# Performance work log

Measured on AMD Instinct MI355X. Metric: run time of the kernel, lower is better.

The kernel has to match this reference:

```python
import jax, jax.numpy as jnp
import numpy as np

N_NODES = 50000
NEG_SLOPE = 0.2


def _gat_conv(x, src, dst, W, a_src, a_dst, b, num_nodes):
    # W: [H*C, F_in]; a_src/a_dst: [H, C]; b: [H*C]
    H, C = a_src.shape
    xp = (x @ W.T).reshape(num_nodes, H, C)              # [N,H,C]
    alpha_s = jnp.sum(xp * a_src[None], axis=-1)          # [N,H]
    alpha_d = jnp.sum(xp * a_dst[None], axis=-1)          # [N,H]
    e = jax.nn.leaky_relu(alpha_s[src] + alpha_d[dst], NEG_SLOPE)  # [E,H]
    # segment softmax over incoming edges of each dst node (self-loops guarantee non-empty segments)
    m = jax.ops.segment_max(e, dst, num_segments=num_nodes)
    e = jnp.exp(e - m[dst])
    s = jax.ops.segment_sum(e, dst, num_segments=num_nodes)
    alpha = e / s[dst]                                    # [E,H]
    out = jax.ops.segment_sum(alpha[:, :, None] * xp[src], dst, num_segments=num_nodes)  # [N,H,C]
    return out.reshape(num_nodes, H * C) + b


def setup_inputs() -> dict:
    key = jax.random.key(0)
    ks = jax.random.split(key, 12)
    N, E, F_in, HID, H, Z = N_NODES, 800000, 128, 64, 2, 32
    sc = 0.1
    return {
        "features": jax.random.normal(ks[0], (N, F_in), jnp.float32),
        "edges": jax.random.randint(ks[1], (2, E), 0, N, jnp.int32),
        "W1": jax.random.normal(ks[2], (H * HID, F_in), jnp.float32) * sc,
        "a_src1": jax.random.normal(ks[3], (H, HID), jnp.float32) * sc,
        "a_dst1": jax.random.normal(ks[4], (H, HID), jnp.float32) * sc,
        "b1": jnp.zeros((H * HID,), jnp.float32),
        "W_mu": jax.random.normal(ks[5], (Z, H * HID), jnp.float32) * sc,
        "a_src_mu": jax.random.normal(ks[6], (1, Z), jnp.float32) * sc,
        "a_dst_mu": jax.random.normal(ks[7], (1, Z), jnp.float32) * sc,
        "b_mu": jnp.zeros((Z,), jnp.float32),
        "W_std": jax.random.normal(ks[8], (Z, H * HID), jnp.float32) * sc,
        "a_src_std": jax.random.normal(ks[9], (1, Z), jnp.float32) * sc,
        "a_dst_std": jax.random.normal(ks[10], (1, Z), jnp.float32) * sc,
        "b_std": jnp.zeros((Z,), jnp.float32),
    }


def reference(features, edges, W1, a_src1, a_dst1, b1, W_mu, a_src_mu, a_dst_mu, b_mu, W_std, a_src_std, a_dst_std, b_std):
    N = features.shape[0]
    loops = jnp.arange(N, dtype=edges.dtype)
    src = jnp.concatenate([edges[0], loops])  # add self loops (PyG default)
    dst = jnp.concatenate([edges[1], loops])
    h = _gat_conv(features, src, dst, W1, a_src1, a_dst1, b1, N)
    h = jax.nn.relu(h)  # dropout p=0.0 -> identity
    mu = _gat_conv(h, src, dst, W_mu, a_src_mu, a_dst_mu, b_mu, N)
    std = _gat_conv(h, src, dst, W_std, a_src_std, a_dst_std, b_std, N)
    return (mu, std)
```

## Files before the change

### kernel.cpp

```cpp
#include <hip/hip_runtime.h>
#include <math.h>

#define N_NODES 50000
#define N_EDGES 800000
#define ET (N_EDGES + N_NODES)
#define KD 128
#define Z 32
#define SH 7
#define BW 128
#define NBUCK ((N_NODES + BW - 1) / BW)
#define CHUNK 4096
#define NBLKA ((ET + CHUNK - 1) / CHUNK)
#define MTOT (NBUCK * NBLKA)
#define MBS ((MTOT + 1023) / 1024)

typedef __attribute__((ext_vector_type(8))) short bf16x8;
typedef __attribute__((ext_vector_type(4))) float f32x4;

static __device__ __forceinline__ float lrelu(float x){ return x > 0.f ? x : 0.2f*x; }
static __device__ __forceinline__ float bf2f(unsigned int u16){ return __uint_as_float(u16 << 16); }
static __device__ __forceinline__ float lof(unsigned int u){ return __uint_as_float(u << 16); }
static __device__ __forceinline__ float hif(unsigned int u){ return __uint_as_float(u & 0xffff0000u); }
static __device__ __forceinline__ unsigned short f2bf(float f){
  unsigned int x = __float_as_uint(f);
  return (unsigned short)((x + 0x7fffu + ((x >> 16) & 1u)) >> 16);
}

__global__ __launch_bounds__(256) void bhistA_kernel(const int* __restrict__ edges, int* __restrict__ M){
  int k = blockIdx.x, t = threadIdx.x;
  __shared__ int cnt[NBUCK];
  for(int b = t; b < NBUCK; b += 256) cnt[b] = 0;
  __syncthreads();
  int base = k*CHUNK;
  int lim = min(base + CHUNK, ET);
  for(int i = base + t; i < lim; i += 256){
    int d = (i < N_EDGES) ? edges[N_EDGES + i] : (i - N_EDGES);
    atomicAdd(&cnt[d >> SH], 1);
  }
  __syncthreads();
  for(int b = t; b < NBUCK; b += 256) M[b*NBLKA + k] = cnt[b];
}

__global__ __launch_bounds__(256) void scanM1_kernel(const int* __restrict__ M, int* __restrict__ bsumM){
  int b = blockIdx.x, t = threadIdx.x;
  int base = b*1024 + t*4;
  int s = 0;
  #pragma unroll
  for(int i=0;i<4;i++){ int n = base+i; if(n < MTOT) s += M[n]; }
  for(int off=32; off; off>>=1) s += __shfl_xor(s, off);
  __shared__ int ws[4];
  if((t&63)==0) ws[t>>6] = s;
  __syncthreads();
  if(t==0) bsumM[b] = ws[0]+ws[1]+ws[2]+ws[3];
}

__global__ __launch_bounds__(256) void scanM2_kernel(const int* __restrict__ bsumM, int* __restrict__ bpreM){
  __shared__ int sm[256];
  int t = threadIdx.x;
  int v = (t < MBS) ? bsumM[t] : 0;
  sm[t] = v;
  __syncthreads();
  for(int off=1; off<256; off<<=1){
    int u = (t >= off) ? sm[t-off] : 0;
    __syncthreads();
    sm[t] += u;
    __syncthreads();
  }
  if(t < MBS) bpreM[t] = sm[t] - v;
}

__global__ __launch_bounds__(256) void scanM3_kernel(const int* __restrict__ M, const int* __restrict__ bpreM,
                                                     int* __restrict__ Mpos){
  int b = blockIdx.x, t = threadIdx.x;
  int lane = t & 63, wv = t >> 6;
  int base = b*1024 + t*4;
  int d[4]; int s = 0;
  #pragma unroll
  for(int i=0;i<4;i++){ int n = base+i; d[i] = (n < MTOT) ? M[n] : 0; s += d[i]; }
  int v = s;
  for(int off=1; off<64; off<<=1){
    int u = __shfl_up(v, off);
    if(lane >= off) v += u;
  }
  int texcl = v - s;
  __shared__ int wtot[4];
  if(lane == 63) wtot[wv] = v;
  __syncthreads();
  int woff = 0;
  for(int i=0;i<wv;i++) woff += wtot[i];
  int run = bpreM[b] + woff + texcl;
  #pragma unroll
  for(int i=0;i<4;i++){
    int n = base+i;
    if(n < MTOT){ Mpos[n] = run; run += d[i]; }
  }
}

__global__ __launch_bounds__(256) void bplaceA_kernel(const int* __restrict__ edges, const int* __restrict__ Mpos,
                                                      int2* __restrict__ etmp){
  int k = blockIdx.x, t = threadIdx.x;
  __shared__ int cur[NBUCK];
  for(int b = t; b < NBUCK; b += 256) cur[b] = Mpos[b*NBLKA + k];
  __syncthreads();
  int base = k*CHUNK;
  int lim = min(base + CHUNK, ET);
  for(int i = base + t; i < lim; i += 256){
    int s, d;
    if(i < N_EDGES){ s = edges[i]; d = edges[N_EDGES+i]; } else { s = d = i - N_EDGES; }
    int pos = atomicAdd(&cur[d >> SH], 1);
    etmp[pos] = make_int2(s, d);
  }
}

__global__ __launch_bounds__(256) void bfin_kernel(const int* __restrict__ Mpos, const int2* __restrict__ etmp,
                                                   int* __restrict__ rowptr, int* __restrict__ esrc){
  int b = blockIdx.x, t = threadIdx.x;
  __shared__ int cnt[BW];
  __shared__ int pre[BW];
  __shared__ int lcur[BW];
  if(t < BW) cnt[t] = 0;
  __syncthreads();
  int beg = Mpos[b*NBLKA];
  int end = (b+1 < NBUCK) ? Mpos[(b+1)*NBLKA] : ET;
  for(int i = beg + t; i < end; i += 256) atomicAdd(&cnt[etmp[i].y & (BW-1)], 1);
  __syncthreads();
  if(t < BW) pre[t] = cnt[t];
  __syncthreads();
  for(int off=1; off<BW; off<<=1){
    int u = 0;
    if(t < BW && t >= off) u = pre[t-off];
    __syncthreads();
    if(t < BW) pre[t] += u;
    __syncthreads();
  }
  if(t < BW){
    int excl = pre[t] - cnt[t];
    int node = b*BW + t;
    if(node < N_NODES) rowptr[node] = beg + excl;
    lcur[t] = beg + excl;
  }
  if(b == 0 && t == 255) rowptr[N_NODES] = ET;
  __syncthreads();
  for(int i = beg + t; i < end; i += 256){
    int2 e = etmp[i];
    int pos = atomicAdd(&lcur[e.y & (BW-1)], 1);
    esrc[pos] = e.x;
  }
}

__global__ __launch_bounds__(256) void wconv_kernel(const float* __restrict__ W1,
                                                    const float* __restrict__ Wmu, const float* __restrict__ Wst,
                                                    unsigned short* __restrict__ Wb1, unsigned short* __restrict__ Wb2){
  int i = blockIdx.x*256 + threadIdx.x;
  if(i < 128*KD) Wb1[i] = f2bf(W1[i]);
  if(i < 64*KD) Wb2[i] = f2bf(i < 32*KD ? Wmu[i] : Wst[i - 32*KD]);
}

__global__ __launch_bounds__(256) void mmt1_kernel(const float* __restrict__ X,
                                                   const unsigned short* __restrict__ Wb,
                                                   const float* __restrict__ asv, const float* __restrict__ adv,
                                                   unsigned short* __restrict__ outb,
                                                   float* __restrict__ as1, float* __restrict__ ad1){
  constexpr int OC = 128, CT = 8;
  int t = threadIdx.x;
  int w = t >> 6, L = t & 63;
  int col = L & 15, quad = L >> 4;
  int row0 = blockIdx.x*64 + w*16;
  int rA = row0 + col;
  if(rA >= N_NODES) rA = N_NODES-1;

  f32x4 acc[CT];
  #pragma unroll
  for(int ct=0;ct<CT;ct++) acc[ct] = (f32x4){0.f,0.f,0.f,0.f};

  #pragma unroll
  for(int kc=0;kc<4;kc++){
    int k0 = kc*32 + quad*8;
    const float* Xf = X + (size_t)rA*KD + k0;
    float4 p = *(const float4*)Xf;
    float4 q = *(const float4*)(Xf + 4);
    bf16x8 a;
    a[0] = (short)f2bf(p.x); a[1] = (short)f2bf(p.y);
    a[2] = (short)f2bf(p.z); a[3] = (short)f2bf(p.w);
    a[4] = (short)f2bf(q.x); a[5] = (short)f2bf(q.y);
    a[6] = (short)f2bf(q.z); a[7] = (short)f2bf(q.w);
    #pragma unroll
    for(int ct=0;ct<CT;ct++){
      bf16x8 b = *(const bf16x8*)(Wb + (size_t)(ct*16 + col)*KD + k0);
      acc[ct] = __builtin_amdgcn_mfma_f32_16x16x32_bf16(a, b, acc[ct], 0, 0, 0);
    }
  }

  float av[CT], dv[CT];
  #pragma unroll
  for(int ct=0;ct<CT;ct++){ av[ct] = asv[ct*16 + col]; dv[ct] = adv[ct*16 + col]; }

  #pragma unroll
  for(int r=0;r<4;r++){
    int row = row0 + quad*4 + r;
    #pragma unroll
    for(int ct=0;ct<CT;ct++)
      if(row < N_NODES) outb[(size_t)row*OC + ct*16 + col] = f2bf(acc[ct][r]);
    float s0 = acc[0][r]*av[0] + acc[1][r]*av[1] + acc[2][r]*av[2] + acc[3][r]*av[3];
    float s1 = acc[4][r]*av[4] + acc[5][r]*av[5] + acc[6][r]*av[6] + acc[7][r]*av[7];
    float d0 = acc[0][r]*dv[0] + acc[1][r]*dv[1] + acc[2][r]*dv[2] + acc[3][r]*dv[3];
    float d1 = acc[4][r]*dv[4] + acc[5][r]*dv[5] + acc[6][r]*dv[6] + acc[7][r]*dv[7];
    #pragma unroll
    for(int off=1; off<16; off<<=1){
      s0 += __shfl_xor(s0, off); s1 += __shfl_xor(s1, off);
      d0 += __shfl_xor(d0, off); d1 += __shfl_xor(d1, off);
    }
    if(col == 0 && row < N_NODES){
      as1[row*2] = s0; as1[row*2+1] = s1;
      ad1[row*2] = d0; ad1[row*2+1] = d1;
    }
  }
}

__global__ __launch_bounds__(256) void mmt2_kernel(const unsigned short* __restrict__ Xb,
                                                   const unsigned short* __restrict__ Wb,
                                                   const float* __restrict__ asmu, const float* __restrict__ admu,
                                                   const float* __restrict__ asst, const float* __restrict__ adst,
                                                   unsigned short* __restrict__ outb,
                                                   float* __restrict__ as2, float* __restrict__ ad2){
  constexpr int OC = 64, CT = 4;
  int t = threadIdx.x;
  int w = t >> 6, L = t & 63;
  int col = L & 15, quad = L >> 4;
  int row0 = blockIdx.x*64 + w*16;
  int rA = row0 + col;
  if(rA >= N_NODES) rA = N_NODES-1;

  f32x4 acc[CT];
  #pragma unroll
  for(int ct=0;ct<CT;ct++) acc[ct] = (f32x4){0.f,0.f,0.f,0.f};

  #pragma unroll
  for(int kc=0;kc<4;kc++){
    int k0 = kc*32 + quad*8;
    bf16x8 a = *(const bf16x8*)(Xb + (size_t)rA*KD + k0);
    #pragma unroll
    for(int ct=0;ct<CT;ct++){
      bf16x8 b = *(const bf16x8*)(Wb + (size_t)(ct*16 + col)*KD + k0);
      acc[ct] = __builtin_amdgcn_mfma_f32_16x16x32_bf16(a, b, acc[ct], 0, 0, 0);
    }
  }

  float av[CT], dv[CT];
  #pragma unroll
  for(int ct=0;ct<CT;ct++){
    av[ct] = (ct < 2) ? asmu[ct*16 + col] : asst[(ct-2)*16 + col];
    dv[ct] = (ct < 2) ? admu[ct*16 + col] : adst[(ct-2)*16 + col];
  }

  #pragma unroll
  for(int r=0;r<4;r++){
    int row = row0 + quad*4 + r;
    #pragma unroll
    for(int ct=0;ct<CT;ct++)
      if(row < N_NODES) outb[(size_t)row*OC + ct*16 + col] = f2bf(acc[ct][r]);
    float smu = acc[0][r]*av[0] + acc[1][r]*av[1];
    float sst = acc[2][r]*av[2] + acc[3][r]*av[3];
    float dmu = acc[0][r]*dv[0] + acc[1][r]*dv[1];
    float dst = acc[2][r]*dv[2] + acc[3][r]*dv[3];
    #pragma unroll
    for(int off=1; off<16; off<<=1){
      smu += __shfl_xor(smu, off); sst += __shfl_xor(sst, off);
      dmu += __shfl_xor(dmu, off); dst += __shfl_xor(dst, off);
    }
    if(col == 0 && row < N_NODES){
      as2[row*2] = smu; as2[row*2+1] = sst;
      ad2[row*2] = dmu; ad2[row*2+1] = dst;
    }
  }
}

__global__ __launch_bounds__(256) void agg1_kernel(const int* __restrict__ rowptr, const int* __restrict__ esrc,
                                                   const float* __restrict__ as1, const float* __restrict__ ad1,
                                                   const unsigned int* __restrict__ xb,
                                                   const float* __restrict__ b1, unsigned int* __restrict__ hb){
  int node = blockIdx.x*4 + (threadIdx.x>>6);
  int l = threadIdx.x & 63;
  if(node >= N_NODES) return;
  int beg = rowptr[node], end = rowptr[node+1];
  const float2* asp = (const float2*)as1;
  float2 adn = ((const float2*)ad1)[node];
  float accx = 0.f, accy = 0.f, s0 = 0.f, s1 = 0.f;
  int n = end - beg;
  int nq = n & ~7;

#define F1_E(j)  int e##j = esrc[i+j];
#define F1_A(j)  float2 a##j = asp[e##j];
#define F1_U(j)  unsigned int u##j = xb[(size_t)e##j*64 + l];
#define F1_C(j)  { float wx = __expf(lrelu(a##j.x + adn.x)); \
                   float wy = __expf(lrelu(a##j.y + adn.y)); \
                   s0 += wx; s1 += wy; \
                   float vv = (l < 32) ? wx : wy; \
                   accx += vv * lof(u##j); accy += vv * hif(u##j); }

  for(int i = beg; i < beg + nq; i += 8){
    F1_E(0) F1_E(1) F1_E(2) F1_E(3) F1_E(4) F1_E(5) F1_E(6) F1_E(7)
    F1_A(0) F1_A(1) F1_A(2) F1_A(3) F1_A(4) F1_A(5) F1_A(6) F1_A(7)
    F1_U(0) F1_U(1) F1_U(2) F1_U(3) F1_U(4) F1_U(5) F1_U(6) F1_U(7)
    F1_C(0) F1_C(1) F1_C(2) F1_C(3) F1_C(4) F1_C(5) F1_C(6) F1_C(7)
  }
  for(int i = beg + nq; i < end; i++){
    F1_E(0) F1_A(0) F1_U(0) F1_C(0)
  }
#undef F1_E
#undef F1_A
#undef F1_U
#undef F1_C
  float sd = (l < 32) ? s0 : s1;
  float2 bb = ((const float2*)b1)[l];
  float rx = fmaxf(accx/sd + bb.x, 0.f);
  float ry = fmaxf(accy/sd + bb.y, 0.f);
  unsigned int hp = (unsigned int)f2bf(rx) | ((unsigned int)f2bf(ry) << 16);
  hb[(size_t)node*64 + l] = hp;
}

__global__ __launch_bounds__(256) void agg2_kernel(const int* __restrict__ rowptr, const int* __restrict__ esrc,
                                                   const float* __restrict__ as2, const float* __restrict__ ad2,
                                                   const uint2* __restrict__ xb2,
                                                   const float* __restrict__ bmu, const float* __restrict__ bst,
                                                   float* __restrict__ out){
  int node = blockIdx.x*4 + (threadIdx.x>>6);
  int l = threadIdx.x & 63;
  if(node >= N_NODES) return;
  int g = l >> 4, c = l & 15;
  int beg = rowptr[node], end = rowptr[node+1];
  const float2* asp = (const float2*)as2;
  float2 adn = ((const float2*)ad2)[node];
  int n = end - beg;
  float a0=0.f, a1=0.f, a2=0.f, a3=0.f, smu=0.f, sst=0.f;
  int nquad = n >> 2;
  int mainq = nquad & ~3;

#define G2(j) int e##j = esrc[base + 4*j]; float2 aa##j = asp[e##j];
#define U2(j) uint2 u##j = xb2[(size_t)e##j*16 + c];
#define C2(j) { float wx = __expf(lrelu(aa##j.x + adn.x)); \
                float wy = __expf(lrelu(aa##j.y + adn.y)); \
                smu += wx; sst += wy; \
                float vv = (c < 8) ? wx : wy; \
                a0 += vv*lof(u##j.x); a1 += vv*hif(u##j.x); \
                a2 += vv*lof(u##j.y); a3 += vv*hif(u##j.y); }

  for(int qq = 0; qq < mainq; qq += 4){
    int base = beg + 4*qq + g;
    G2(0) G2(1) G2(2) G2(3)
    U2(0) U2(1) U2(2) U2(3)
    C2(0) C2(1) C2(2) C2(3)
  }
  for(int qq = mainq; qq < nquad; qq++){
    int base = beg + 4*qq + g;
    G2(0) U2(0) C2(0)
  }
  int tail = n & 3;
  if(g < tail){
    int idx = beg + 4*nquad + g;
    int e = esrc[idx];
    float2 aa = asp[e];
    uint2 u = xb2[(size_t)e*16 + c];
    float wx = __expf(lrelu(aa.x + adn.x));
    float wy = __expf(lrelu(aa.y + adn.y));
    smu += wx; sst += wy;
    float vv = (c < 8) ? wx : wy;
    a0 += vv*lof(u.x); a1 += vv*hif(u.x);
    a2 += vv*lof(u.y); a3 += vv*hif(u.y);
  }
#undef G2
#undef U2
#undef C2
  #pragma unroll
  for(int off = 16; off < 64; off <<= 1){
    smu += __shfl_xor(smu, off); sst += __shfl_xor(sst, off);
    a0 += __shfl_xor(a0, off); a1 += __shfl_xor(a1, off);
    a2 += __shfl_xor(a2, off); a3 += __shfl_xor(a3, off);
  }
  float sd = (c < 8) ? smu : sst;
  float4 bb = (c < 8) ? *(const float4*)(bmu + 4*c) : *(const float4*)(bst + 4*(c-8));
  float4 r;
  r.x = a0/sd + bb.x;
  r.y = a1/sd + bb.y;
  r.z = a2/sd + bb.z;
  r.w = a3/sd + bb.w;
  if(g == 0){
    float* dst = (c < 8) ? (out + (size_t)node*Z + 4*c)
                         : (out + (size_t)N_NODES*Z + (size_t)node*Z + 4*(c-8));
    *(float4*)dst = r;
  }
}

extern "C" void kernel_launch(void* const* d_in, const int* in_sizes, int n_in,
                              void* d_out, int out_size, void* d_ws, size_t ws_size,
                              hipStream_t stream){
  const float* x    = (const float*)d_in[0];
  const int*   edges= (const int*)d_in[1];
  const float* W1   = (const float*)d_in[2];
  const float* as1v = (const float*)d_in[3];
  const float* ad1v = (const float*)d_in[4];
  const float* b1   = (const float*)d_in[5];
  const float* Wmu  = (const float*)d_in[6];
  const float* asmu = (const float*)d_in[7];
  const float* admu = (const float*)d_in[8];
  const float* bmu  = (const float*)d_in[9];
  const float* Wst  = (const float*)d_in[10];
  const float* asst = (const float*)d_in[11];
  const float* adst = (const float*)d_in[12];
  const float* bst  = (const float*)d_in[13];
  float* out = (float*)d_out;

  char* p = (char*)d_ws;
  auto alloc = [&](size_t bytes)->char*{ char* r = p; p += (bytes + 255) & ~size_t(255); return r; };
  int*   M      = (int*)  alloc((size_t)MTOT*4);
  int*   Mpos   = (int*)  alloc((size_t)MTOT*4);
  int*   bsumM  = (int*)  alloc((size_t)MBS*4);
  int*   bpreM  = (int*)  alloc((size_t)MBS*4);
  int2*  etmp   = (int2*) alloc((size_t)ET*8);
  int*   esrc   = (int*)  alloc((size_t)ET*4);
  int*   rowptr = (int*)  alloc((size_t)(N_NODES+1)*4);
  unsigned short* Wb1 = (unsigned short*)alloc((size_t)128*KD*2);
  unsigned short* Wb2 = (unsigned short*)alloc((size_t)64*KD*2);
  unsigned short* xpb1 = (unsigned short*)alloc((size_t)N_NODES*128*2);
  float* as1    = (float*)alloc((size_t)N_NODES*2*4);
  float* ad1    = (float*)alloc((size_t)N_NODES*2*4);
  unsigned short* hb = (unsigned short*)alloc((size_t)N_NODES*128*2);
  float* as2    = (float*)alloc((size_t)N_NODES*2*4);
  float* ad2    = (float*)alloc((size_t)N_NODES*2*4);
  unsigned short* xpb2 = xpb1;

  bhistA_kernel  <<<NBLKA, 256, 0, stream>>>(edges, M);
  scanM1_kernel  <<<MBS, 256, 0, stream>>>(M, bsumM);
  scanM2_kernel  <<<1, 256, 0, stream>>>(bsumM, bpreM);
  scanM3_kernel  <<<MBS, 256, 0, stream>>>(M, bpreM, Mpos);
  bplaceA_kernel <<<NBLKA, 256, 0, stream>>>(edges, Mpos, etmp);
  bfin_kernel    <<<NBUCK, 256, 0, stream>>>(Mpos, etmp, rowptr, esrc);

  wconv_kernel   <<<(128*KD + 255)/256, 256, 0, stream>>>(W1, Wmu, Wst, Wb1, Wb2);

  mmt1_kernel <<<(N_NODES+63)/64, 256, 0, stream>>>(x, Wb1, as1v, ad1v, xpb1, as1, ad1);
  agg1_kernel <<<(N_NODES+3)/4, 256, 0, stream>>>(rowptr, esrc, as1, ad1, (const unsigned int*)xpb1, b1, (unsigned int*)hb);

  mmt2_kernel <<<(N_NODES+63)/64, 256, 0, stream>>>(hb, Wb2, asmu, admu, asst, adst, xpb1, as2, ad2);
  agg2_kernel <<<(N_NODES+3)/4, 256, 0, stream>>>(rowptr, esrc, as2, ad2, (const uint2*)xpb2, bmu, bst, out);
}
```

Before: 248.9 us.

## Precompute per-edge attention weights in a separate pass before aggregation

Adds a wcalc kernel that computes exp(leaky_relu(a_src[s]+a_dst[d])) for every edge into a buffer that reuses the etmp workspace. bfin now also writes a destination array to feed it. The aggregation kernels then read one contiguous float2 weight per edge instead of gathering a_src and running exp, which removes a random gather and 64x-redundant exp work per wave. The cost is two extra kernel launches and extra memory traffic: edst is written, and the weights are written and read again.

After: 252.9 us. About the same (+1.6%).

```diff
diff --git a/kernel.cpp b/kernel.cpp
--- a/kernel.cpp
+++ b/kernel.cpp
@@ -113,7 +113,8 @@
 }
 
 __global__ __launch_bounds__(256) void bfin_kernel(const int* __restrict__ Mpos, const int2* __restrict__ etmp,
-                                                   int* __restrict__ rowptr, int* __restrict__ esrc){
+                                                   int* __restrict__ rowptr, int* __restrict__ esrc,
+                                                   int* __restrict__ edst){
   int b = blockIdx.x, t = threadIdx.x;
   __shared__ int cnt[BW];
   __shared__ int pre[BW];
@@ -145,6 +146,7 @@
     int2 e = etmp[i];
     int pos = atomicAdd(&lcur[e.y & (BW-1)], 1);
     esrc[pos] = e.x;
+    edst[pos] = e.y;
   }
 }
 
@@ -275,40 +277,47 @@
   }
 }
 
+__global__ __launch_bounds__(256) void wcalc_kernel(const int* __restrict__ esrc, const int* __restrict__ edst,
+                                                    const float* __restrict__ as, const float* __restrict__ ad,
+                                                    float2* __restrict__ wp){
+  int i = blockIdx.x*256 + threadIdx.x;
+  if(i >= ET) return;
+  int s = esrc[i], d = edst[i];
+  float2 a = ((const float2*)as)[s];
+  float2 b = ((const float2*)ad)[d];
+  wp[i] = make_float2(__expf(lrelu(a.x + b.x)), __expf(lrelu(a.y + b.y)));
+}
+
 __global__ __launch_bounds__(256) void agg1_kernel(const int* __restrict__ rowptr, const int* __restrict__ esrc,
-                                                   const float* __restrict__ as1, const float* __restrict__ ad1,
+                                                   const float2* __restrict__ wp,
                                                    const unsigned int* __restrict__ xb,
                                                    const float* __restrict__ b1, unsigned int* __restrict__ hb){
   int node = blockIdx.x*4 + (threadIdx.x>>6);
   int l = threadIdx.x & 63;
   if(node >= N_NODES) return;
   int beg = rowptr[node], end = rowptr[node+1];
-  const float2* asp = (const float2*)as1;
-  float2 adn = ((const float2*)ad1)[node];
   float accx = 0.f, accy = 0.f, s0 = 0.f, s1 = 0.f;
   int n = end - beg;
   int nq = n & ~7;
 
 #define F1_E(j)  int e##j = esrc[i+j];
-#define F1_A(j)  float2 a##j = asp[e##j];
+#define F1_W(j)  float2 w##j = wp[i+j];
 #define F1_U(j)  unsigned int u##j = xb[(size_t)e##j*64 + l];
-#define F1_C(j)  { float wx = __expf(lrelu(a##j.x + adn.x)); \
-                   float wy = __expf(lrelu(a##j.y + adn.y)); \
-                   s0 += wx; s1 += wy; \
-                   float vv = (l < 32) ? wx : wy; \
+#define F1_C(j)  { s0 += w##j.x; s1 += w##j.y; \
+                   float vv = (l < 32) ? w##j.x : w##j.y; \
                    accx += vv * lof(u##j); accy += vv * hif(u##j); }
 
   for(int i = beg; i < beg + nq; i += 8){
     F1_E(0) F1_E(1) F1_E(2) F1_E(3) F1_E(4) F1_E(5) F1_E(6) F1_E(7)
-    F1_A(0) F1_A(1) F1_A(2) F1_A(3) F1_A(4) F1_A(5) F1_A(6) F1_A(7)
+    F1_W(0) F1_W(1) F1_W(2) F1_W(3) F1_W(4) F1_W(5) F1_W(6) F1_W(7)
     F1_U(0) F1_U(1) F1_U(2) F1_U(3) F1_U(4) F1_U(5) F1_U(6) F1_U(7)
     F1_C(0) F1_C(1) F1_C(2) F1_C(3) F1_C(4) F1_C(5) F1_C(6) F1_C(7)
   }
   for(int i = beg + nq; i < end; i++){
-    F1_E(0) F1_A(0) F1_U(0) F1_C(0)
+    F1_E(0) F1_W(0) F1_U(0) F1_C(0)
   }
 #undef F1_E
-#undef F1_A
+#undef F1_W
 #undef F1_U
 #undef F1_C
   float sd = (l < 32) ? s0 : s1;
@@ -320,7 +329,7 @@
 }
 
 __global__ __launch_bounds__(256) void agg2_kernel(const int* __restrict__ rowptr, const int* __restrict__ esrc,
-                                                   const float* __restrict__ as2, const float* __restrict__ ad2,
+                                                   const float2* __restrict__ wp,
                                                    const uint2* __restrict__ xb2,
                                                    const float* __restrict__ bmu, const float* __restrict__ bst,
                                                    float* __restrict__ out){
@@ -329,19 +338,15 @@
   if(node >= N_NODES) return;
   int g = l >> 4, c = l & 15;
   int beg = rowptr[node], end = rowptr[node+1];
-  const float2* asp = (const float2*)as2;
-  float2 adn = ((const float2*)ad2)[node];
   int n = end - beg;
   float a0=0.f, a1=0.f, a2=0.f, a3=0.f, smu=0.f, sst=0.f;
   int nquad = n >> 2;
   int mainq = nquad & ~3;
 
-#define G2(j) int e##j = esrc[base + 4*j]; float2 aa##j = asp[e##j];
+#define G2(j) int e##j = esrc[base + 4*j]; float2 w##j = wp[base + 4*j];
 #define U2(j) uint2 u##j = xb2[(size_t)e##j*16 + c];
-#define C2(j) { float wx = __expf(lrelu(aa##j.x + adn.x)); \
-                float wy = __expf(lrelu(aa##j.y + adn.y)); \
-                smu += wx; sst += wy; \
-                float vv = (c < 8) ? wx : wy; \
+#define C2(j) { smu += w##j.x; sst += w##j.y; \
+                float vv = (c < 8) ? w##j.x : w##j.y; \
                 a0 += vv*lof(u##j.x); a1 += vv*hif(u##j.x); \
                 a2 += vv*lof(u##j.y); a3 += vv*hif(u##j.y); }
 
@@ -359,12 +364,10 @@
   if(g < tail){
     int idx = beg + 4*nquad + g;
     int e = esrc[idx];
-    float2 aa = asp[e];
+    float2 w = wp[idx];
     uint2 u = xb2[(size_t)e*16 + c];
-    float wx = __expf(lrelu(aa.x + adn.x));
-    float wy = __expf(lrelu(aa.y + adn.y));
-    smu += wx; sst += wy;
-    float vv = (c < 8) ? wx : wy;
+    smu += w.x; sst += w.y;
+    float vv = (c < 8) ? w.x : w.y;
     a0 += vv*lof(u.x); a1 += vv*hif(u.x);
     a2 += vv*lof(u.y); a3 += vv*hif(u.y);
   }
@@ -418,6 +421,7 @@
   int*   bpreM  = (int*)  alloc((size_t)MBS*4);
   int2*  etmp   = (int2*) alloc((size_t)ET*8);
   int*   esrc   = (int*)  alloc((size_t)ET*4);
+  int*   edst   = (int*)  alloc((size_t)ET*4);
   int*   rowptr = (int*)  alloc((size_t)(N_NODES+1)*4);
   unsigned short* Wb1 = (unsigned short*)alloc((size_t)128*KD*2);
   unsigned short* Wb2 = (unsigned short*)alloc((size_t)64*KD*2);
@@ -428,19 +432,22 @@
   float* as2    = (float*)alloc((size_t)N_NODES*2*4);
   float* ad2    = (float*)alloc((size_t)N_NODES*2*4);
   unsigned short* xpb2 = xpb1;
+  float2* wedge = (float2*)etmp;
 
   bhistA_kernel  <<<NBLKA, 256, 0, stream>>>(edges, M);
   scanM1_kernel  <<<MBS, 256, 0, stream>>>(M, bsumM);
   scanM2_kernel  <<<1, 256, 0, stream>>>(bsumM, bpreM);
   scanM3_kernel  <<<MBS, 256, 0, stream>>>(M, bpreM, Mpos);
   bplaceA_kernel <<<NBLKA, 256, 0, stream>>>(edges, Mpos, etmp);
-  bfin_kernel    <<<NBUCK, 256, 0, stream>>>(Mpos, etmp, rowptr, esrc);
+  bfin_kernel    <<<NBUCK, 256, 0, stream>>>(Mpos, etmp, rowptr, esrc, edst);
 
   wconv_kernel   <<<(128*KD + 255)/256, 256, 0, stream>>>(W1, Wmu, Wst, Wb1, Wb2);
 
-  mmt1_kernel <<<(N_NODES+63)/64, 256, 0, stream>>>(x, Wb1, as1v, ad1v, xpb1, as1, ad1);
-  agg1_kernel <<<(N_NODES+3)/4, 256, 0, stream>>>(rowptr, esrc, as1, ad1, (const unsigned int*)xpb1, b1, (unsigned int*)hb);
-
-  mmt2_kernel <<<(N_NODES+63)/64, 256, 0, stream>>>(hb, Wb2, asmu, admu, asst, adst, xpb1, as2, ad2);
-  agg2_kernel <<<(N_NODES+3)/4, 256, 0, stream>>>(rowptr, esrc, as2, ad2, (const uint2*)xpb2, bmu, bst, out);
-}
+  mmt1_kernel  <<<(N_NODES+63)/64, 256, 0, stream>>>(x, Wb1, as1v, ad1v, xpb1, as1, ad1);
+  wcalc_kernel <<<(ET+255)/256, 256, 0, stream>>>(esrc, edst, as1, ad1, wedge);
+  agg1_kernel  <<<(N_NODES+3)/4, 256, 0, stream>>>(rowptr, esrc, wedge, (const unsigned int*)xpb1, b1, (unsigned int*)hb);
+
+  mmt2_kernel  <<<(N_NODES+63)/64, 256, 0, stream>>>(hb, Wb2, asmu, admu, asst, adst, xpb1, as2, ad2);
+  wcalc_kernel <<<(ET+255)/256, 256, 0, stream>>>(esrc, edst, as2, ad2, wedge);
+  agg2_kernel  <<<(N_NODES+3)/4, 256, 0, stream>>>(rowptr, esrc, wedge, (const uint2*)xpb2, bmu, bst, out);
+}
```
